# Kernel optimization log

Measured on AMD Instinct MI355X. Metric: run time of the kernel, lower is better.

## Reference

```python
import jax, jax.numpy as jnp
import numpy as np

ALPHA = 0.2  # LeakyReLU negative slope


def setup_inputs() -> dict:
    key = jax.random.key(0)
    k1, k2 = jax.random.split(key)
    B, W, K = 32, 128, 1024
    x = jax.random.normal(k1, (B, W, K), dtype=jnp.float32)
    # xavier_uniform with gain=1.414 on shape (2W, 1)
    fan_in, fan_out = 2 * W, 1
    bound = 1.414 * np.sqrt(6.0 / (fan_in + fan_out))
    w = jax.random.uniform(k2, (2 * W, 1), dtype=jnp.float32, minval=-bound, maxval=bound)
    return {"x": x, "w": w}


def reference(x, w):
    # x: (B, W, K) -> v: (B, K, W)
    v = jnp.transpose(x, (0, 2, 1))
    Wdim = v.shape[-1]
    # concat(v_i, v_j) @ w  ==  v_i @ w[:W] + v_j @ w[W:]
    w1 = w[:Wdim, 0]  # (W,)
    w2 = w[Wdim:, 0]  # (W,)
    s1 = v @ w1  # (B, K)
    s2 = v @ w2  # (B, K)
    e = jax.nn.leaky_relu(s1[:, :, None] + s2[:, None, :], negative_slope=ALPHA)  # (B, K, K)
    attention = jax.nn.softmax(e, axis=2)
    # dropout=0.0 / eval mode -> identity
    h = jnp.einsum('bij,bjw->biw', attention, v)  # (B, K, W)
    return h
```

## Files before the change

kernel.cpp:

```cpp
#include <hip/hip_runtime.h>

#define ALPHA 0.2f

constexpr int WDIM = 128;
constexpr int KDIM = 1024;
constexpr int NSEG = 64;
constexpr int SEGLEN = KDIM / NSEG;

typedef _Float16 h4 __attribute__((ext_vector_type(4)));
typedef _Float16 h8 __attribute__((ext_vector_type(8)));

constexpr int OFF_XTH  = 0;
constexpr int OFF_TABH = 32768;
constexpr int OFF_ESC  = 163968;
constexpr int OFF_ESCA = 164992;
constexpr int OFF_ABT  = 166016;
constexpr int OFF_U    = 168192;
constexpr int OFF_T    = 169216;
constexpr int OFF_S1   = 170240;
constexpr int OFF_S2   = 171264;
constexpr int OFF_CC   = 172288;
constexpr int OFF_PERM = 173312;
constexpr int OFF_TA   = 174336;
constexpr int OFF_TB   = 182528;
constexpr int OFF_SBA  = 190720;
constexpr int OFF_SBB  = 198912;
constexpr int PBF      = 207104;

__global__ __launch_bounds__(256) void k_s12(const float* __restrict__ x,
                                             const float* __restrict__ w,
                                             float* __restrict__ ws, int b0) {
  const int slot = blockIdx.y;
  const int b = b0 + slot;
  float* base = ws + (size_t)slot * PBF;
  __shared__ float w1s[WDIM], w2s[WDIM];
  __shared__ float red1[4][64], red2[4][64];
  int t = threadIdx.x;
  if (t < WDIM) { w1s[t] = w[t]; w2s[t] = w[WDIM + t]; }
  __syncthreads();
  int jj = t & 63, wg = t >> 6;
  int j = blockIdx.x * 64 + jj;
  int w0 = wg * 32;
  const float* xb = x + (size_t)b * (WDIM * KDIM);
  float s1 = 0.f, s2 = 0.f;
  float vals[32];
#pragma unroll
  for (int k = 0; k < 32; ++k) {
    float v = xb[(w0 + k) * KDIM + j];
    vals[k] = v;
    s1 = fmaf(v, w1s[w0 + k], s1);
    s2 = fmaf(v, w2s[w0 + k], s2);
  }
  _Float16* xrowh = (_Float16*)(base + OFF_XTH) + j * WDIM + w0;
#pragma unroll
  for (int q = 0; q < 4; ++q) {
    h8 hv;
#pragma unroll
    for (int e = 0; e < 8; ++e) hv[e] = (_Float16)vals[8 * q + e];
    *(h8*)(xrowh + 8 * q) = hv;
  }
  red1[wg][jj] = s1;
  red2[wg][jj] = s2;
  __syncthreads();
  if (wg == 0) {
    base[OFF_S1 + j] = red1[0][jj] + red1[1][jj] + red1[2][jj] + red1[3][jj];
    base[OFF_S2 + j] = red2[0][jj] + red2[1][jj] + red2[2][jj] + red2[3][jj];
  }
}

__global__ __launch_bounds__(512) void k_rank(float* __restrict__ ws) {
  const int slot = blockIdx.y;
  float* base = ws + (size_t)slot * PBF;
  __shared__ float s2s[KDIM];
  __shared__ float red[512];
  __shared__ int pr[128][4], pc[128][4];
  int t = threadIdx.x;
  for (int i = t; i < KDIM; i += 512) s2s[i] = base[OFF_S2 + i];
  __syncthreads();
  red[t] = fmaxf(s2s[t], s2s[t + 512]);
  __syncthreads();
  for (int s = 256; s > 0; s >>= 1) {
    if (t < s) red[t] = fmaxf(red[t], red[t + s]);
    __syncthreads();
  }
  float M2 = red[0];
  int jj = t >> 2, quarter = t & 3;
  int j = blockIdx.x * 128 + jj;
  float s2me = s2s[j];
  float s1me = base[OFF_S1 + j];
  float key = -s1me;
  int r = 0, c = 0;
  int lo = quarter * 256;
#pragma unroll 4
  for (int k2 = 0; k2 < 256; ++k2) {
    float v = s2s[lo + k2];
    int jp = lo + k2;
    r += (v > s2me || (v == s2me && jp < j)) ? 1 : 0;
    c += (v >= key) ? 1 : 0;
  }
  pr[jj][quarter] = r;
  pc[jj][quarter] = c;
  __syncthreads();
  if (quarter == 0) {
    int R = pr[jj][0] + pr[jj][1] + pr[jj][2] + pr[jj][3];
    int C = pc[jj][0] + pc[jj][1] + pc[jj][2] + pc[jj][3];
    ((int*)(base + OFF_CC))[j] = C;
    ((int*)(base + OFF_PERM))[R] = j;
    base[OFF_ESC + R] = __expf(s2me - M2);
    base[OFF_ESCA + R] = __expf(ALPHA * s2me);
    float z = s1me + M2;
    float mi = z >= 0.f ? z : ALPHA * z;
    base[OFF_U + j] = __expf(z - mi);
    base[OFF_T + j] = __expf(ALPHA * s1me - mi);
  }
}

__global__ __launch_bounds__(256) void k_tot(float* __restrict__ ws) {
  const int slot = blockIdx.y;
  float* base = ws + (size_t)slot * PBF;
  __shared__ float sc[256];
  int t = threadIdx.x;
  int bx = blockIdx.x;
  if (bx < 32) {
    int w = t & 127, sl = t >> 7;
    int seg = bx * 2 + sl;
    int r0 = seg * SEGLEN;
    const _Float16* xTh = (const _Float16*)(base + OFF_XTH);
    const int* prm = (const int*)(base + OFF_PERM);
    int pr16[SEGLEN];
#pragma unroll
    for (int k = 0; k < SEGLEN; ++k) pr16[k] = prm[r0 + k];
    float xv[SEGLEN], eav[SEGLEN], ebv[SEGLEN];
#pragma unroll
    for (int k = 0; k < SEGLEN; ++k) {
      xv[k] = (float)xTh[pr16[k] * WDIM + w];
      eav[k] = base[OFF_ESC + r0 + k];
      ebv[k] = base[OFF_ESCA + r0 + k];
    }
    float ta = 0.f, tb = 0.f;
#pragma unroll
    for (int k = 0; k < SEGLEN; ++k) {
      ta = fmaf(eav[k], xv[k], ta);
      tb = fmaf(ebv[k], xv[k], tb);
    }
    base[OFF_TA + seg * WDIM + w] = ta;
    base[OFF_TB + seg * WDIM + w] = tb;
  } else if (bx == 32) {
    float4 v = *(const float4*)(base + OFF_ESC + 4 * t);
    float p1 = v.x, p2 = p1 + v.y, p3 = p2 + v.z, p4 = p3 + v.w;
    sc[t] = p4;
    __syncthreads();
    for (int s = 1; s < 256; s <<= 1) {
      float add = (t >= s) ? sc[t - s] : 0.f;
      __syncthreads();
      sc[t] += add;
      __syncthreads();
    }
    float bs = (t > 0) ? sc[t - 1] : 0.f;
    float* ABT = base + OFF_ABT;
    ABT[2 * (4 * t + 1)] = bs + p1;
    ABT[2 * (4 * t + 2)] = bs + p2;
    ABT[2 * (4 * t + 3)] = bs + p3;
    ABT[2 * (4 * t + 4)] = bs + p4;
    if (t == 0) ABT[0] = 0.f;
  } else {
    float4 v = *(const float4*)(base + OFF_ESCA + 4 * t);
    float q3 = v.w, q2 = v.z + q3, q1 = v.y + q2, q0 = v.x + q1;
    sc[t] = q0;
    __syncthreads();
    for (int s = 1; s < 256; s <<= 1) {
      float add = (t + s < 256) ? sc[t + s] : 0.f;
      __syncthreads();
      sc[t] += add;
      __syncthreads();
    }
    float bs = (t < 255) ? sc[t + 1] : 0.f;
    float* ABT = base + OFF_ABT;
    ABT[2 * (4 * t + 0) + 1] = bs + q0;
    ABT[2 * (4 * t + 1) + 1] = bs + q1;
    ABT[2 * (4 * t + 2) + 1] = bs + q2;
    ABT[2 * (4 * t + 3) + 1] = bs + q3;
    if (t == 255) ABT[2 * KDIM + 1] = 0.f;
  }
}

__global__ __launch_bounds__(256) void k_base(float* __restrict__ ws) {
  float* base = ws + (size_t)blockIdx.x * PBF;
  __shared__ float gA[2][128], gB[2][128];
  int t = threadIdx.x;
  int w = t & 127, h = t >> 7;
  float ta32[32], tb32[32];
  float ga = 0.f, gb = 0.f;
#pragma unroll
  for (int k = 0; k < 32; ++k) {
    ta32[k] = base[OFF_TA + (h * 32 + k) * WDIM + w];
    tb32[k] = base[OFF_TB + (h * 32 + k) * WDIM + w];
    ga += ta32[k];
    gb += tb32[k];
  }
  gA[h][w] = ga;
  gB[h][w] = gb;
  __syncthreads();
  float bA = (h == 1) ? gA[0][w] : 0.f;
  float bB = (h == 0) ? gB[1][w] : 0.f;
#pragma unroll
  for (int k = 0; k < 32; ++k) {
    base[OFF_SBA + (h * 32 + k) * WDIM + w] = bA;
    bA += ta32[k];
  }
#pragma unroll
  for (int k = 31; k >= 0; --k) {
    base[OFF_SBB + (h * 32 + k) * WDIM + w] = bB;
    bB += tb32[k];
  }
}

__global__ __launch_bounds__(128) void k_scan(float* __restrict__ ws) {
  const int slot = blockIdx.y;
  float* base = ws + (size_t)slot * PBF;
  int seg = blockIdx.x;
  int wl = threadIdx.x;
  int r0 = seg * SEGLEN;
  const _Float16* xTh = (const _Float16*)(base + OFF_XTH);
  const int* prm = (const int*)(base + OFF_PERM);
  int pr16[SEGLEN];
#pragma unroll
  for (int k = 0; k < SEGLEN; ++k) pr16[k] = prm[r0 + k];
  float xv[SEGLEN], eav[SEGLEN], ebv[SEGLEN];
#pragma unroll
  for (int k = 0; k < SEGLEN; ++k) {
    xv[k] = (float)xTh[pr16[k] * WDIM + wl];
    eav[k] = base[OFF_ESC + r0 + k];
    ebv[k] = base[OFF_ESCA + r0 + k];
  }
  _Float16* TABh = (_Float16*)(base + OFF_TABH);
  float accA = 0.f;
#pragma unroll
  for (int k = 0; k < SEGLEN; ++k) {
    TABh[(r0 + k) * 256 + wl] = (_Float16)accA;
    accA = fmaf(eav[k], xv[k], accA);
  }
  if (seg == NSEG - 1) {
    TABh[KDIM * 256 + wl] = (_Float16)accA;
    TABh[KDIM * 256 + 128 + wl] = (_Float16)0.f;
  }
  float accB = 0.f;
#pragma unroll
  for (int k = SEGLEN - 1; k >= 0; --k) {
    accB = fmaf(ebv[k], xv[k], accB);
    TABh[(r0 + k) * 256 + 128 + wl] = (_Float16)accB;
  }
}

__global__ __launch_bounds__(256) void k_out(const float* __restrict__ ws,
                                             float* __restrict__ out, int b0) {
  const int slot = blockIdx.y;
  const int b = b0 + slot;
  const float* base = ws + (size_t)slot * PBF;
  int q = blockIdx.x * 256 + threadIdx.x;
  int i = q >> 5;
  int wq = (q & 31) << 2;
  int c = ((const int*)(base + OFF_CC))[i];
  int seg = c >> 4; if (seg > NSEG - 1) seg = NSEG - 1;
  float u = base[OFF_U + i];
  float tt = base[OFF_T + i];
  float2 ab = *(const float2*)(base + OFF_ABT + 2 * c);
  float rden = 1.f / fmaf(u, ab.x, tt * ab.y);
  const _Float16* TABh = (const _Float16*)(base + OFF_TABH);
  h4 A4 = *(const h4*)(TABh + (size_t)c * 256 + wq);
  h4 B4 = *(const h4*)(TABh + (size_t)c * 256 + 128 + wq);
  float4 sa4 = *(const float4*)(base + OFF_SBA + seg * WDIM + wq);
  float4 sb4 = *(const float4*)(base + OFF_SBB + seg * WDIM + wq);
  float4 o;
  o.x = (u * (sa4.x + (float)A4[0]) + tt * (sb4.x + (float)B4[0])) * rden;
  o.y = (u * (sa4.y + (float)A4[1]) + tt * (sb4.y + (float)B4[1])) * rden;
  o.z = (u * (sa4.z + (float)A4[2]) + tt * (sb4.z + (float)B4[2])) * rden;
  o.w = (u * (sa4.w + (float)A4[3]) + tt * (sb4.w + (float)B4[3])) * rden;
  *(float4*)(out + (size_t)b * (KDIM * WDIM) + (size_t)q * 4) = o;
}

extern "C" void kernel_launch(void* const* d_in, const int* in_sizes, int n_in,
                              void* d_out, int out_size, void* d_ws, size_t ws_size,
                              hipStream_t stream) {
  const float* x = (const float*)d_in[0];
  const float* w = (const float*)d_in[1];
  float* out = (float*)d_out;
  float* ws = (float*)d_ws;
  const int NB = 32;
  size_t perb = (size_t)PBF * sizeof(float);
  int nbmax = (int)(ws_size / perb);
  if (nbmax < 1) nbmax = 1;
  if (nbmax > NB) nbmax = NB;
  for (int b0 = 0; b0 < NB; b0 += nbmax) {
    int nb = (NB - b0 < nbmax) ? (NB - b0) : nbmax;
    k_s12<<<dim3(16, nb), 256, 0, stream>>>(x, w, ws, b0);
    k_rank<<<dim3(8, nb), 512, 0, stream>>>(ws);
    k_tot<<<dim3(34, nb), 256, 0, stream>>>(ws);
    k_base<<<nb, 256, 0, stream>>>(ws);
    k_scan<<<dim3(NSEG, nb), 128, 0, stream>>>(ws);
    k_out<<<dim3(128, nb), 256, 0, stream>>>(ws, out, b0);
  }
}
```

Before: 49.07 us.

## Fuse segment totals into scan kernel and merge prefix passes into base kernel

The segment scan kernel now writes each segment's final A/B totals as a by-product of its local scans. This replaces the separate totals pass that re-gathered x and recomputed the same sums. The base-offset computation and the two exp-prefix scans are merged into one three-block kernel, cutting the launch sequence from six kernels to five per batch chunk. k_out must now add segment base offsets (SBA/SBB) to the locally scanned TABh values. That part of k_out is not shown, so correctness depends on it already doing so.

```diff
diff --git a/kernel.cpp b/kernel.cpp
--- a/kernel.cpp
+++ b/kernel.cpp
@@ -115,37 +115,77 @@
   }
 }
 
-__global__ __launch_bounds__(256) void k_tot(float* __restrict__ ws) {
+__global__ __launch_bounds__(128) void k_scant(float* __restrict__ ws) {
   const int slot = blockIdx.y;
   float* base = ws + (size_t)slot * PBF;
+  int seg = blockIdx.x;
+  int wl = threadIdx.x;
+  int r0 = seg * SEGLEN;
+  const _Float16* xTh = (const _Float16*)(base + OFF_XTH);
+  const int* prm = (const int*)(base + OFF_PERM);
+  int pr16[SEGLEN];
+#pragma unroll
+  for (int k = 0; k < SEGLEN; ++k) pr16[k] = prm[r0 + k];
+  float xv[SEGLEN], eav[SEGLEN], ebv[SEGLEN];
+#pragma unroll
+  for (int k = 0; k < SEGLEN; ++k) {
+    xv[k] = (float)xTh[pr16[k] * WDIM + wl];
+    eav[k] = base[OFF_ESC + r0 + k];
+    ebv[k] = base[OFF_ESCA + r0 + k];
+  }
+  _Float16* TABh = (_Float16*)(base + OFF_TABH);
+  float accA = 0.f;
+#pragma unroll
+  for (int k = 0; k < SEGLEN; ++k) {
+    TABh[(r0 + k) * 256 + wl] = (_Float16)accA;
+    accA = fmaf(eav[k], xv[k], accA);
+  }
+  base[OFF_TA + seg * WDIM + wl] = accA;
+  if (seg == NSEG - 1) {
+    TABh[KDIM * 256 + wl] = (_Float16)accA;
+    TABh[KDIM * 256 + 128 + wl] = (_Float16)0.f;
+  }
+  float accB = 0.f;
+#pragma unroll
+  for (int k = SEGLEN - 1; k >= 0; --k) {
+    accB = fmaf(ebv[k], xv[k], accB);
+    TABh[(r0 + k) * 256 + 128 + wl] = (_Float16)accB;
+  }
+  base[OFF_TB + seg * WDIM + wl] = accB;
+}
+
+__global__ __launch_bounds__(256) void k_base(float* __restrict__ ws) {
+  float* base = ws + (size_t)blockIdx.y * PBF;
+  __shared__ float gA[2][128], gB[2][128];
   __shared__ float sc[256];
   int t = threadIdx.x;
-  int bx = blockIdx.x;
-  if (bx < 32) {
-    int w = t & 127, sl = t >> 7;
-    int seg = bx * 2 + sl;
-    int r0 = seg * SEGLEN;
-    const _Float16* xTh = (const _Float16*)(base + OFF_XTH);
-    const int* prm = (const int*)(base + OFF_PERM);
-    int pr16[SEGLEN];
-#pragma unroll
-    for (int k = 0; k < SEGLEN; ++k) pr16[k] = prm[r0 + k];
-    float xv[SEGLEN], eav[SEGLEN], ebv[SEGLEN];
-#pragma unroll
-    for (int k = 0; k < SEGLEN; ++k) {
-      xv[k] = (float)xTh[pr16[k] * WDIM + w];
-      eav[k] = base[OFF_ESC + r0 + k];
-      ebv[k] = base[OFF_ESCA + r0 + k];
-    }
-    float ta = 0.f, tb = 0.f;
-#pragma unroll
-    for (int k = 0; k < SEGLEN; ++k) {
-      ta = fmaf(eav[k], xv[k], ta);
-      tb = fmaf(ebv[k], xv[k], tb);
-    }
-    base[OFF_TA + seg * WDIM + w] = ta;
-    base[OFF_TB + seg * WDIM + w] = tb;
-  } else if (bx == 32) {
+  if (blockIdx.x == 0) {
+    int w = t & 127, h = t >> 7;
+    float ta32[32], tb32[32];
+    float ga = 0.f, gb = 0.f;
+#pragma unroll
+    for (int k = 0; k < 32; ++k) {
+      ta32[k] = base[OFF_TA + (h * 32 + k) * WDIM + w];
+      tb32[k] = base[OFF_TB + (h * 32 + k) * WDIM + w];
+      ga += ta32[k];
+      gb += tb32[k];
+    }
+    gA[h][w] = ga;
+    gB[h][w] = gb;
+    __syncthreads();
+    float bA = (h == 1) ? gA[0][w] : 0.f;
+    float bB = (h == 0) ? gB[1][w] : 0.f;
+#pragma unroll
+    for (int k = 0; k < 32; ++k) {
+      base[OFF_SBA + (h * 32 + k) * WDIM + w] = bA;
+      bA += ta32[k];
+    }
+#pragma unroll
+    for (int k = 31; k >= 0; --k) {
+      base[OFF_SBB + (h * 32 + k) * WDIM + w] = bB;
+      bB += tb32[k];
+    }
+  } else if (blockIdx.x == 1) {
     float4 v = *(const float4*)(base + OFF_ESC + 4 * t);
     float p1 = v.x, p2 = p1 + v.y, p3 = p2 + v.z, p4 = p3 + v.w;
     sc[t] = p4;
@@ -181,74 +221,6 @@
     ABT[2 * (4 * t + 2) + 1] = bs + q2;
     ABT[2 * (4 * t + 3) + 1] = bs + q3;
     if (t == 255) ABT[2 * KDIM + 1] = 0.f;
-  }
-}
-
-__global__ __launch_bounds__(256) void k_base(float* __restrict__ ws) {
-  float* base = ws + (size_t)blockIdx.x * PBF;
-  __shared__ float gA[2][128], gB[2][128];
-  int t = threadIdx.x;
-  int w = t & 127, h = t >> 7;
-  float ta32[32], tb32[32];
-  float ga = 0.f, gb = 0.f;
-#pragma unroll
-  for (int k = 0; k < 32; ++k) {
-    ta32[k] = base[OFF_TA + (h * 32 + k) * WDIM + w];
-    tb32[k] = base[OFF_TB + (h * 32 + k) * WDIM + w];
-    ga += ta32[k];
-    gb += tb32[k];
-  }
-  gA[h][w] = ga;
-  gB[h][w] = gb;
-  __syncthreads();
-  float bA = (h == 1) ? gA[0][w] : 0.f;
-  float bB = (h == 0) ? gB[1][w] : 0.f;
-#pragma unroll
-  for (int k = 0; k < 32; ++k) {
-    base[OFF_SBA + (h * 32 + k) * WDIM + w] = bA;
-    bA += ta32[k];
-  }
-#pragma unroll
-  for (int k = 31; k >= 0; --k) {
-    base[OFF_SBB + (h * 32 + k) * WDIM + w] = bB;
-    bB += tb32[k];
-  }
-}
-
-__global__ __launch_bounds__(128) void k_scan(float* __restrict__ ws) {
-  const int slot = blockIdx.y;
-  float* base = ws + (size_t)slot * PBF;
-  int seg = blockIdx.x;
-  int wl = threadIdx.x;
-  int r0 = seg * SEGLEN;
-  const _Float16* xTh = (const _Float16*)(base + OFF_XTH);
-  const int* prm = (const int*)(base + OFF_PERM);
-  int pr16[SEGLEN];
-#pragma unroll
-  for (int k = 0; k < SEGLEN; ++k) pr16[k] = prm[r0 + k];
-  float xv[SEGLEN], eav[SEGLEN], ebv[SEGLEN];
-#pragma unroll
-  for (int k = 0; k < SEGLEN; ++k) {
-    xv[k] = (float)xTh[pr16[k] * WDIM + wl];
-    eav[k] = base[OFF_ESC + r0 + k];
-    ebv[k] = base[OFF_ESCA + r0 + k];
-  }
-  _Float16* TABh = (_Float16*)(base + OFF_TABH);
-  float accA = 0.f;
-#pragma unroll
-  for (int k = 0; k < SEGLEN; ++k) {
-    TABh[(r0 + k) * 256 + wl] = (_Float16)accA;
-    accA = fmaf(eav[k], xv[k], accA);
-  }
-  if (seg == NSEG - 1) {
-    TABh[KDIM * 256 + wl] = (_Float16)accA;
-    TABh[KDIM * 256 + 128 + wl] = (_Float16)0.f;
-  }
-  float accB = 0.f;
-#pragma unroll
-  for (int k = SEGLEN - 1; k >= 0; --k) {
-    accB = fmaf(ebv[k], xv[k], accB);
-    TABh[(r0 + k) * 256 + 128 + wl] = (_Float16)accB;
   }
 }
 
@@ -295,9 +267,8 @@
     int nb = (NB - b0 < nbmax) ? (NB - b0) : nbmax;
     k_s12<<<dim3(16, nb), 256, 0, stream>>>(x, w, ws, b0);
     k_rank<<<dim3(8, nb), 512, 0, stream>>>(ws);
-    k_tot<<<dim3(34, nb), 256, 0, stream>>>(ws);
-    k_base<<<nb, 256, 0, stream>>>(ws);
-    k_scan<<<dim3(NSEG, nb), 128, 0, stream>>>(ws);
+    k_scant<<<dim3(NSEG, nb), 128, 0, stream>>>(ws);
+    k_base<<<dim3(3, nb), 256, 0, stream>>>(ws);
     k_out<<<dim3(128, nb), 256, 0, stream>>>(ws, out, b0);
   }
 }
```

Measured after the change: 44.67 us. 9.0% less time.
